# Kernel tuning notes

Measured on AMD Instinct MI355X. Metric: run time of the kernel, lower is better.

Reference implementation:

```python
import jax, jax.numpy as jnp
import numpy as np
from jax import lax

D_MODEL = 60
D_INNER = 120   # expand=2
D_STATE = 16
D_CONV = 4
DT_RANK = 4     # ceil(60/16)
DEPTH = 2
BATCH = 2
H_IMG = 128
W_IMG = 128
L_SEQ = H_IMG * W_IMG


def setup_inputs() -> dict:
    key = jax.random.key(0)
    ks = jax.random.split(key, 12)
    s = 0.02
    x = jax.random.normal(ks[0], (BATCH, L_SEQ, D_MODEL), jnp.float32)
    ln_w = jnp.ones((DEPTH, D_MODEL), jnp.float32)
    ln_b = jnp.zeros((DEPTH, D_MODEL), jnp.float32)
    in_proj_w = jax.random.normal(ks[1], (DEPTH, 2 * D_INNER, D_MODEL), jnp.float32) * s
    conv_w = jax.random.normal(ks[2], (DEPTH, D_INNER, D_CONV), jnp.float32) * s
    conv_b = jnp.zeros((DEPTH, D_INNER), jnp.float32)
    x_proj_w = jax.random.normal(ks[3], (DEPTH, DT_RANK + 2 * D_STATE, D_INNER), jnp.float32) * s
    dt_proj_w = jax.random.normal(ks[4], (DEPTH, D_INNER, DT_RANK), jnp.float32) * s
    dt_proj_b = jnp.full((DEPTH, D_INNER), -4.0, jnp.float32)  # softplus^-1 of small dt
    A_log = jnp.broadcast_to(
        jnp.log(jnp.arange(1, D_STATE + 1, dtype=jnp.float32))[None, None, :],
        (DEPTH, D_INNER, D_STATE)).copy()
    D_skip = jnp.ones((DEPTH, D_INNER), jnp.float32)
    out_proj_w = jax.random.normal(ks[5], (DEPTH, D_MODEL, D_INNER), jnp.float32) * s
    conv2d_w = jax.random.normal(ks[6], (D_MODEL, D_MODEL, 3, 3), jnp.float32) * s
    conv2d_b = jnp.zeros((D_MODEL,), jnp.float32)
    return {"x": x, "ln_w": ln_w, "ln_b": ln_b, "in_proj_w": in_proj_w,
            "conv_w": conv_w, "conv_b": conv_b, "x_proj_w": x_proj_w,
            "dt_proj_w": dt_proj_w, "dt_proj_b": dt_proj_b, "A_log": A_log,
            "D": D_skip, "out_proj_w": out_proj_w,
            "conv2d_w": conv2d_w, "conv2d_b": conv2d_b,
            "H": H_IMG, "W": W_IMG}


def _layernorm(x, w, b, eps=1e-5):
    mu = jnp.mean(x, axis=-1, keepdims=True)
    var = jnp.mean(jnp.square(x - mu), axis=-1, keepdims=True)
    return (x - mu) * lax.rsqrt(var + eps) * w + b


def _selective_scan(dA, dBx, C):
    # dA, dBx: [B, L, D_INNER, D_STATE]; C: [B, L, D_STATE]
    def step(h, inp):
        dA_t, dBx_t, c_t = inp
        h = dA_t * h + dBx_t                       # [B, D_INNER, D_STATE]
        y = jnp.einsum('bdn,bn->bd', h, c_t)
        return h, y
    h0 = jnp.zeros(dA.shape[:1] + dA.shape[2:], dA.dtype)
    _, ys = lax.scan(step, h0,
                     (dA.transpose(1, 0, 2, 3), dBx.transpose(1, 0, 2, 3),
                      C.transpose(1, 0, 2)))
    return ys.transpose(1, 0, 2)                    # [B, L, D_INNER]


def _mamba(x, in_w, cw, cb, xp_w, dtw, dtb, A_log, D_skip, out_w):
    # x: [B, L, D_MODEL]
    xz = jnp.einsum('bld,ed->ble', x, in_w)         # [B, L, 2*D_INNER]
    xin, z = jnp.split(xz, 2, axis=-1)
    # causal depthwise conv1d over L
    xc = xin.transpose(0, 2, 1)                     # [B, D_INNER, L]
    xc = jnp.pad(xc, ((0, 0), (0, 0), (D_CONV - 1, 0)))
    xc = lax.conv_general_dilated(xc, cw[:, None, :], (1,), 'VALID',
                                  dimension_numbers=('NCH', 'OIH', 'NCH'),
                                  feature_group_count=D_INNER)
    xc = jax.nn.silu(xc + cb[None, :, None]).transpose(0, 2, 1)  # [B, L, D_INNER]
    xdb = jnp.einsum('bld,ed->ble', xc, xp_w)       # [B, L, DT_RANK + 2*D_STATE]
    dt = xdb[..., :DT_RANK]
    Bm = xdb[..., DT_RANK:DT_RANK + D_STATE]
    Cm = xdb[..., DT_RANK + D_STATE:]
    delta = jax.nn.softplus(jnp.einsum('blr,dr->bld', dt, dtw) + dtb)  # [B, L, D_INNER]
    A = -jnp.exp(A_log)                              # [D_INNER, D_STATE]
    dA = jnp.exp(delta[..., None] * A[None, None])   # [B, L, D_INNER, D_STATE]
    dBx = delta[..., None] * Bm[:, :, None, :] * xc[..., None]
    y = _selective_scan(dA, dBx, Cm) + D_skip * xc
    y = y * jax.nn.silu(z)
    return jnp.einsum('ble,de->bld', y, out_w)       # [B, L, D_MODEL]


def reference(x, ln_w, ln_b, in_proj_w, conv_w, conv_b, x_proj_w,
              dt_proj_w, dt_proj_b, A_log, D, out_proj_w,
              conv2d_w, conv2d_b, H, W):
    h = x
    for i in range(DEPTH):
        hn = _layernorm(h, ln_w[i], ln_b[i])
        h = _mamba(hn, in_proj_w[i], conv_w[i], conv_b[i], x_proj_w[i],
                   dt_proj_w[i], dt_proj_b[i], A_log[i], D[i], out_proj_w[i])
    # patch_unembed -> 3x3 conv -> patch_embed, residual add (RMMB)
    b = h.shape[0]
    img = h.transpose(0, 2, 1).reshape(b, D_MODEL, H, W)
    img = lax.conv_general_dilated(img, conv2d_w, (1, 1), 'SAME',
                                   dimension_numbers=('NCHW', 'OIHW', 'NCHW'))
    img = img + conv2d_b[None, :, None, None]
    h = img.reshape(b, D_MODEL, H * W).transpose(0, 2, 1)
    return h + x
```

## Files before the change

kernel.cpp:

```cpp
#include <hip/hip_runtime.h>
#include <math.h>

#define BATCH 2
#define LSEQ 16384
#define DM 60
#define DI 120
#define NCH 512
#define TCH 32
#define HH 128
#define WW 128

typedef __attribute__((ext_vector_type(8))) short bhalf8;
typedef __attribute__((ext_vector_type(4))) short short4v;
typedef __attribute__((ext_vector_type(4))) float f32x4;

__device__ __forceinline__ float sigmoidf_(float x){ return __builtin_amdgcn_rcpf(1.0f + __expf(-x)); }
__device__ __forceinline__ float siluf_(float x){ return x * sigmoidf_(x); }
__device__ __forceinline__ float softplusf_(float x){ return (x > 20.0f) ? x : __logf(1.0f + __expf(x)); }
__device__ __forceinline__ short f2b(float f){
  union{float f; unsigned u;} v; v.f = f;
  unsigned r = (v.u + 0x7fffu + ((v.u >> 16) & 1u)) >> 16;
  return (short)r;
}
__device__ __forceinline__ float b2f(short s){
  union{float f; unsigned u;} v; v.u = ((unsigned)(unsigned short)s) << 16; return v.f;
}

__device__ __forceinline__ void powers16(float r, float* dA){
  dA[0] = r;
  #pragma unroll
  for (int n = 1; n < 16; n++) dA[n] = dA[(n-1)>>1] * dA[n>>1];
}
__device__ __forceinline__ void powers8(float r, float* p){
  p[0] = r;
  #pragma unroll
  for (int n = 1; n < 8; n++) p[n] = p[(n-1)>>1] * p[n>>1];
}

__global__ __launch_bounds__(256) void k_pack(
    const float* __restrict__ ipw, const float* __restrict__ xpw,
    const float* __restrict__ opw,
    const float* __restrict__ lnw, const float* __restrict__ lnb,
    short* __restrict__ pk, float* __restrict__ c01)
{
  int i = blockIdx.x*256 + threadIdx.x;
  if (i < 2*240*64){
    int l = i / (240*64);
    int rem = i % (240*64);
    int n = rem / 64, k = rem % 64;
    float v = (k < 60) ? ipw[(size_t)l*14400 + n*60 + k] * lnw[l*60 + k] : 0.f;
    pk[i] = f2b(v);
  } else if (i < 30720 + 2*48*128){
    int j = i - 30720;
    int l = j / (48*128);
    int rem = j % (48*128);
    int n = rem / 128, k = rem % 128;
    float v = (n < 36 && k < 120) ? xpw[(size_t)l*36*120 + n*120 + k] : 0.f;
    pk[i] = f2b(v);
  } else if (i < 43008 + 480){
    int j = i - 43008;
    int l = j / 240, n = j % 240;
    float c1 = 0.f, c0 = 0.f;
    for (int k = 0; k < 60; k++){
      float w = ipw[(size_t)l*14400 + n*60 + k];
      c1 += lnw[l*60+k] * w;
      c0 += lnb[l*60+k] * w;
    }
    c01[(l*240 + n)*2 + 0] = c1;
    c01[(l*240 + n)*2 + 1] = c0;
  } else if (i < 43488 + 2*64*128){
    int j = i - 43488;
    int l = j / 8192;
    int rem = j % 8192;
    int n = rem / 128, k = rem % 128;
    float v = (n < 60 && k < 120) ? opw[(size_t)l*7200 + n*120 + k] : 0.f;
    pk[43008 + j] = f2b(v);
  }
}

__global__ __launch_bounds__(256) void k_lnxp(
    const float* __restrict__ srcf, const short* __restrict__ srcb,
    const short* __restrict__ ipB,
    const float* __restrict__ c01,
    const float* __restrict__ cw, const float* __restrict__ cb,
    const short* __restrict__ xpB,
    const float* __restrict__ dtw, const float* __restrict__ dtb,
    const float* __restrict__ A_log,
    short* __restrict__ zs, short* __restrict__ xcg,
    short* __restrict__ delta, short* __restrict__ BCg,
    float* __restrict__ ap, float* __restrict__ he)
{
  __shared__ __align__(16) char smem[31552];
  short* XB   = (short*)smem;
  short* xcB  = (short*)smem;
  short* xinB = (short*)(smem + 8704);
  float* BLf  = (float*)(smem + 21760);
  short* BCL  = (short*)(smem + 23808);
  float* stats= (float*)(smem + 25856);
  float* dtsh = (float*)(smem + 26240);
  float* cwL  = (float*)(smem + 26752);
  float* Wd5T = (float*)(smem + 28672);
  float* cbL  = (float*)(smem + 30592);
  float* bdL  = (float*)(smem + 31072);
  const int tid = threadIdx.x;
  const int wave = tid >> 6, lane = tid & 63;
  const int m = lane & 15, quad = lane >> 4;
  const int row0 = blockIdx.x * 32;
  const int seq0 = (row0 / LSEQ) * LSEQ;
  for (int i = tid; i < 480; i += 256){ cwL[i] = cw[i]; Wd5T[(i & 3)*120 + (i >> 2)] = dtw[i]; }
  for (int i = tid; i < 120; i += 256){ cbL[i] = cb[i]; bdL[i] = dtb[i]; }
  for (int i = tid; i < 48*16; i += 256){
    int r = i >> 4, g = i & 15;
    int grow = row0 - 3 + r;
    short4v o = {0,0,0,0};
    if (g < 15 && r < 35 && grow >= seq0){
      if (srcb){
        o = *(const short4v*)&srcb[(size_t)grow*60 + g*4];
      } else {
        float4 f = *(const float4*)&srcf[(size_t)grow*60 + g*4];
        o.x = f2b(f.x); o.y = f2b(f.y); o.z = f2b(f.z); o.w = f2b(f.w);
      }
    }
    *(short4v*)&XB[r*72 + g*4] = o;
  }
  __syncthreads();
  {
    const int sub = lane >> 4;
    const int li  = lane & 15;
    #pragma unroll
    for (int it = 0; it < 3; it++){
      int r = it*16 + wave*4 + sub;
      short4v x4 = *(const short4v*)&XB[r*72 + li*4];
      float f0 = b2f(x4.x), f1 = b2f(x4.y), f2 = b2f(x4.z), f3 = b2f(x4.w);
      float sx = (f0 + f1) + (f2 + f3);
      float sq = (f0*f0 + f1*f1) + (f2*f2 + f3*f3);
      #pragma unroll
      for (int off = 1; off < 16; off <<= 1){
        sx += __shfl_xor(sx, off);
        sq += __shfl_xor(sq, off);
      }
      if (li == 0){
        float mu = sx * (1.0f/60.0f);
        float var = fmaxf(sq * (1.0f/60.0f) - mu*mu, 0.f);
        stats[r*2 + 0] = mu;
        stats[r*2 + 1] = rsqrtf(var + 1e-5f);
      }
    }
  }
  __syncthreads();
  for (int t = wave; t < 45; t += 4){
    int mtile = t / 15, ntile = t % 15;
    f32x4 acc = {0.f,0.f,0.f,0.f};
    #pragma unroll
    for (int ks = 0; ks < 2; ks++){
      bhalf8 a = *(const bhalf8*)&XB[(mtile*16 + m)*72 + ks*32 + quad*8];
      bhalf8 b = *(const bhalf8*)&ipB[(ntile*16 + m)*64 + ks*32 + quad*8];
      acc = __builtin_amdgcn_mfma_f32_16x16x32_bf16(a, b, acc, 0, 0, 0);
    }
    int n = ntile*16 + m;
    float2 cc = *(const float2*)&c01[n*2];
    float c1v = cc.x, c0v = cc.y;
    #pragma unroll
    for (int reg = 0; reg < 4; reg++){
      int r = mtile*16 + quad*4 + reg;
      int grow = row0 - 3 + r;
      bool valid = (r < 35) && (grow >= seq0);
      float mu = stats[r*2], rs = stats[r*2+1];
      float val = rs*(acc[reg] - mu*c1v) + c0v;
      if (!valid) val = 0.f;
      if (n < 120){
        xinB[r*136 + n] = f2b(val);
      } else if (r >= 3 && r < 35){
        zs[(size_t)(row0 - 3 + r)*120 + (n - 120)] = f2b(siluf_(val));
      }
    }
  }
  __syncthreads();
  for (int i = tid; i < 960; i += 256){
    int r = i/30, c4 = (i%30)*4;
    float4 cbv = *(const float4*)&cbL[c4];
    float4 w0 = *(const float4*)&cwL[(c4+0)*4];
    float4 w1 = *(const float4*)&cwL[(c4+1)*4];
    float4 w2 = *(const float4*)&cwL[(c4+2)*4];
    float4 w3 = *(const float4*)&cwL[(c4+3)*4];
    short4v x0 = *(const short4v*)&xinB[(r+0)*136 + c4];
    short4v x1 = *(const short4v*)&xinB[(r+1)*136 + c4];
    short4v x2 = *(const short4v*)&xinB[(r+2)*136 + c4];
    short4v x3 = *(const short4v*)&xinB[(r+3)*136 + c4];
    float a0 = cbv.x + w0.x*b2f(x0.x) + w0.y*b2f(x1.x) + w0.z*b2f(x2.x) + w0.w*b2f(x3.x);
    float a1 = cbv.y + w1.x*b2f(x0.y) + w1.y*b2f(x1.y) + w1.z*b2f(x2.y) + w1.w*b2f(x3.y);
    float a2 = cbv.z + w2.x*b2f(x0.z) + w2.y*b2f(x1.z) + w2.z*b2f(x2.z) + w2.w*b2f(x3.z);
    float a3 = cbv.w + w3.x*b2f(x0.w) + w3.y*b2f(x1.w) + w3.z*b2f(x2.w) + w3.w*b2f(x3.w);
    short4v o;
    o.x = f2b(siluf_(a0)); o.y = f2b(siluf_(a1)); o.z = f2b(siluf_(a2)); o.w = f2b(siluf_(a3));
    *(short4v*)&xcB[r*136 + c4] = o;
  }
  for (int i = tid; i < 32*8; i += 256)
    xcB[(i >> 3)*136 + 120 + (i & 7)] = 0;
  __syncthreads();
  for (int t = wave; t < 6; t += 4){
    int mtile = t / 3, ntile = t % 3;
    f32x4 acc = {0.f,0.f,0.f,0.f};
    #pragma unroll
    for (int ks = 0; ks < 4; ks++){
      bhalf8 a = *(const bhalf8*)&xcB[(mtile*16 + m)*136 + ks*32 + quad*8];
      bhalf8 b = *(const bhalf8*)&xpB[(ntile*16 + m)*128 + ks*32 + quad*8];
      acc = __builtin_amdgcn_mfma_f32_16x16x32_bf16(a, b, acc, 0, 0, 0);
    }
    int n = ntile*16 + m;
    #pragma unroll
    for (int reg = 0; reg < 4; reg++){
      int r = mtile*16 + quad*4 + reg;
      float val = acc[reg];
      if (n < 4)        dtsh[r*4 + n] = val;
      else if (n < 36){
        BCL[r*32 + (n - 4)] = f2b(val);
        if (n < 20) BLf[r*16 + (n - 4)] = val;
      }
    }
  }
  __syncthreads();
  for (int i = tid; i < 960; i += 256){
    int row = i/30, c4 = (i%30)*4;
    float4 t4 = *(const float4*)&dtsh[row*4];
    float4 w0 = *(const float4*)&Wd5T[0*120 + c4];
    float4 w1 = *(const float4*)&Wd5T[1*120 + c4];
    float4 w2 = *(const float4*)&Wd5T[2*120 + c4];
    float4 w3 = *(const float4*)&Wd5T[3*120 + c4];
    float4 bb = *(const float4*)&bdL[c4];
    short4v o;
    o.x = f2b(softplusf_(bb.x + t4.x*w0.x + t4.y*w1.x + t4.z*w2.x + t4.w*w3.x));
    o.y = f2b(softplusf_(bb.y + t4.x*w0.y + t4.y*w1.y + t4.z*w2.y + t4.w*w3.y));
    o.z = f2b(softplusf_(bb.z + t4.x*w0.z + t4.y*w1.z + t4.z*w2.z + t4.w*w3.z));
    o.w = f2b(softplusf_(bb.w + t4.x*w0.w + t4.y*w1.w + t4.z*w2.w + t4.w*w3.w));
    *(short4v*)&delta[(size_t)(row0 + row)*120 + c4] = o;
  }
  for (int i = tid; i < 960; i += 256){
    int r = i/30, off = (i%30)*4;
    *(short4v*)&xcg[(size_t)(row0 + r)*120 + off] = *(const short4v*)&xcB[r*136 + off];
  }
  for (int i = tid; i < 256; i += 256)
    *(short4v*)&BCg[(size_t)row0*32 + i*4] = *(const short4v*)&BCL[i*4];
  if (tid < 240){
    const int d = tid >> 1, half = tid & 1, n0 = half*8;
    const int b = row0 / LSEQ;
    const int cglob = (row0 % LSEQ) >> 5;
    float A2[8], h[8];
    const float A20 = -__expf(A_log[d*16]) * 1.44269504f;
    #pragma unroll
    for (int n = 0; n < 8; n++){
      A2[n] = -__expf(A_log[d*16 + n0 + n]) * 1.44269504f;
      h[n] = 0.f;
    }
    bool fastp = true;
    #pragma unroll
    for (int n = 0; n < 8; n++)
      fastp = fastp && (fabsf(A2[n] - (n0+n+1)*A20) <= 1e-4f*fabsf(A2[n]));
    const float w0 = Wd5T[d], w1 = Wd5T[120+d], w2 = Wd5T[240+d], w3 = Wd5T[360+d];
    const float bd = bdL[d];
    int base = (cglob*BATCH + b)*(DI*16) + d*16 + n0;
    if (fastp){
      float P = 1.f;
      for (int t = 0; t < 32; t++){
        float4 t4 = *(const float4*)&dtsh[t*4];
        float del = softplusf_(bd + t4.x*w0 + t4.y*w1 + t4.z*w2 + t4.w*w3);
        float xcv = b2f(xcB[t*136 + d]);
        float dx = del * xcv;
        float r = exp2f(del * A20);
        P *= r;
        float p8[8]; powers8(r, p8);
        float s = half ? p8[7] : 1.0f;
        float4 b0 = *(const float4*)&BLf[t*16 + n0];
        float4 b1 = *(const float4*)&BLf[t*16 + n0 + 4];
        h[0] = (s*p8[0])*h[0] + dx*b0.x;  h[1] = (s*p8[1])*h[1] + dx*b0.y;
        h[2] = (s*p8[2])*h[2] + dx*b0.z;  h[3] = (s*p8[3])*h[3] + dx*b0.w;
        h[4] = (s*p8[4])*h[4] + dx*b1.x;  h[5] = (s*p8[5])*h[5] + dx*b1.y;
        h[6] = (s*p8[6])*h[6] + dx*b1.z;  h[7] = (s*p8[7])*h[7] + dx*b1.w;
      }
      float pp[8]; powers8(P, pp);
      float sP = half ? pp[7] : 1.0f;
      float apv[8];
      #pragma unroll
      for (int j = 0; j < 8; j++) apv[j] = sP*pp[j];
      *(float4*)&ap[base]     = *(float4*)&apv[0];
      *(float4*)&ap[base + 4] = *(float4*)&apv[4];
      *(float4*)&he[base]     = *(float4*)&h[0];
      *(float4*)&he[base + 4] = *(float4*)&h[4];
    } else {
      float apv[8];
      #pragma unroll
      for (int n = 0; n < 8; n++) apv[n] = 1.f;
      for (int t = 0; t < 32; t++){
        float4 t4 = *(const float4*)&dtsh[t*4];
        float del = softplusf_(bd + t4.x*w0 + t4.y*w1 + t4.z*w2 + t4.w*w3);
        float dx = del * b2f(xcB[t*136 + d]);
        #pragma unroll
        for (int n = 0; n < 8; n++){
          float dA = exp2f(del * A2[n]);
          apv[n] *= dA;
          h[n] = dA*h[n] + dx*BLf[t*16 + n0 + n];
        }
      }
      *(float4*)&ap[base]     = *(float4*)&apv[0];
      *(float4*)&ap[base + 4] = *(float4*)&apv[4];
      *(float4*)&he[base]     = *(float4*)&h[0];
      *(float4*)&he[base + 4] = *(float4*)&h[4];
    }
  }
}

__global__ __launch_bounds__(256) void k_scan2(float* __restrict__ ap, const float* __restrict__ he)
{
  __shared__ float aggA[16*17];
  __shared__ float aggB[16*17];
  const int tid = threadIdx.x;
  const int n = tid & 15, j = tid >> 4;
  const int sbase = blockIdx.x*16 + n;
  const int stride = BATCH*DI*16;
  {
    float A = 1.f, B = 0.f;
    int idx = (j*32)*stride + sbase;
    #pragma unroll 4
    for (int k = 0; k < 32; k++){
      float a = ap[idx], h = he[idx];
      B = a*B + h;
      A *= a;
      idx += stride;
    }
    aggA[n*17 + j] = A;
    aggB[n*17 + j] = B;
  }
  __syncthreads();
  if (tid < 16){
    float B = 0.f;
    #pragma unroll
    for (int jj = 0; jj < 16; jj++){
      float Af = aggA[tid*17 + jj];
      float Bf = aggB[tid*17 + jj];
      aggB[tid*17 + jj] = B;
      B = Af*B + Bf;
    }
  }
  __syncthreads();
  {
    float H = aggB[n*17 + j];
    int idx = (j*32)*stride + sbase;
    #pragma unroll 4
    for (int k = 0; k < 32; k++){
      float a = ap[idx], h = he[idx];
      ap[idx] = H;
      H = a*H + h;
      idx += stride;
    }
  }
}

__global__ __launch_bounds__(256) void k_scan3o(
    const short* __restrict__ delta, const short* __restrict__ xc,
    const short* __restrict__ BCg, const short* __restrict__ zs,
    const float* __restrict__ h0, const float* __restrict__ A_log,
    const float* __restrict__ Dsk, const short* __restrict__ opB,
    short* __restrict__ hout)
{
  __shared__ float BCl[TCH*32];
  __shared__ __align__(16) short yL[TCH*136];
  const int tid = threadIdx.x;
  const int wave = tid >> 6, lane = tid & 63;
  const int m = lane & 15, quad = lane >> 4;
  const int c = blockIdx.x % NCH, b = blockIdx.x / NCH;
  const size_t rowbase = (size_t)b*LSEQ + (size_t)c*TCH;
  for (int i = tid; i < TCH*8; i += 256){
    short4v v = *(const short4v*)&BCg[rowbase*32 + i*4];
    float4 f; f.x = b2f(v.x); f.y = b2f(v.y); f.z = b2f(v.z); f.w = b2f(v.w);
    *(float4*)&BCl[i*4] = f;
  }
  for (int i = tid; i < TCH*4; i += 256){
    short4v z = {0,0,0,0};
    *(short4v*)&yL[(i >> 2)*136 + 120 + (i & 3)*4] = z;
  }
  __syncthreads();
  if (tid < 240){
    const int d = tid >> 1, half = tid & 1, n0 = half << 3;
    float A2[8], h[8];
    const int base = (c*BATCH + b)*(DI*16) + d*16 + n0;
    const float A20 = -__expf(A_log[d*16]) * 1.44269504f;
    #pragma unroll
    for (int n = 0; n < 8; n++){
      A2[n] = -__expf(A_log[d*16 + n0 + n]) * 1.44269504f;
      h[n] = h0[base + n];
    }
    bool fastp = true;
    #pragma unroll
    for (int n = 0; n < 8; n++)
      fastp = fastp && (fabsf(A2[n] - (n0+n+1)*A20) <= 1e-4f*fabsf(A2[n]));
    int fp = fastp ? 1 : 0;
    fp &= __shfl_xor(fp, 1);
    const float Dv = Dsk[d];
    if (fp){
      for (int t = 0; t < TCH; t++){
        float del = b2f(delta[(rowbase+t)*DI + d]);
        float xcv = b2f(xc[(rowbase+t)*DI + d]);
        float zv  = b2f(zs[(rowbase+t)*DI + d]);
        float dx = del * xcv;
        float r = exp2f(del * A20);
        float p8[8]; powers8(r, p8);
        float s = half ? p8[7] : 1.0f;
        float4 b0 = *(const float4*)&BCl[t*32 + n0];
        float4 b1 = *(const float4*)&BCl[t*32 + n0 + 4];
        h[0] = (s*p8[0])*h[0] + dx*b0.x;  h[1] = (s*p8[1])*h[1] + dx*b0.y;
        h[2] = (s*p8[2])*h[2] + dx*b0.z;  h[3] = (s*p8[3])*h[3] + dx*b0.w;
        h[4] = (s*p8[4])*h[4] + dx*b1.x;  h[5] = (s*p8[5])*h[5] + dx*b1.y;
        h[6] = (s*p8[6])*h[6] + dx*b1.z;  h[7] = (s*p8[7])*h[7] + dx*b1.w;
        float4 c0 = *(const float4*)&BCl[t*32 + 16 + n0];
        float4 c1 = *(const float4*)&BCl[t*32 + 20 + n0];
        float acc = h[0]*c0.x + h[1]*c0.y + h[2]*c0.z + h[3]*c0.w
                  + h[4]*c1.x + h[5]*c1.y + h[6]*c1.z + h[7]*c1.w;
        acc += __shfl_xor(acc, 1);
        if (!half) yL[t*136 + d] = f2b((acc + Dv*xcv) * zv);
      }
    } else {
      for (int t = 0; t < TCH; t++){
        float del = b2f(delta[(rowbase+t)*DI + d]);
        float xcv = b2f(xc[(rowbase+t)*DI + d]);
        float zv  = b2f(zs[(rowbase+t)*DI + d]);
        float dx = del * xcv;
        float acc = 0.f;
        #pragma unroll
        for (int n = 0; n < 8; n++){
          float dA = exp2f(del * A2[n]);
          h[n] = dA*h[n] + dx*BCl[t*32 + n0 + n];
          acc += h[n]*BCl[t*32 + 16 + n0 + n];
        }
        acc += __shfl_xor(acc, 1);
        if (!half) yL[t*136 + d] = f2b((acc + Dv*xcv) * zv);
      }
    }
  }
  __syncthreads();
  for (int t = wave; t < 8; t += 4){
    const int mtile = t >> 2, ntile = t & 3;
    f32x4 acc = {0.f,0.f,0.f,0.f};
    #pragma unroll
    for (int ks = 0; ks < 4; ks++){
      bhalf8 a  = *(const bhalf8*)&yL[(mtile*16 + m)*136 + ks*32 + quad*8];
      bhalf8 bb = *(const bhalf8*)&opB[(ntile*16 + m)*128 + ks*32 + quad*8];
      acc = __builtin_amdgcn_mfma_f32_16x16x32_bf16(a, bb, acc, 0, 0, 0);
    }
    const int n = ntile*16 + m;
    if (n < 60){
      #pragma unroll
      for (int reg = 0; reg < 4; reg++){
        int r = mtile*16 + quad*4 + reg;
        hout[(rowbase + r)*60 + n] = f2b(acc[reg]);
      }
    }
  }
}

__global__ __launch_bounds__(256) void k_wB(const float* __restrict__ w, short* __restrict__ wB)
{
  int i = blockIdx.x*256 + threadIdx.x;
  if (i >= 9*64*64) return;
  int ci = i & 63, co = (i >> 6) & 63, tap = i >> 12;
  float v = 0.f;
  if (co < 60 && ci < 60) v = w[((size_t)co*60 + ci)*9 + tap];
  wB[i] = f2b(v);
}

__global__ __launch_bounds__(256) void k_conv2d(
    const short* __restrict__ hin, const short* __restrict__ wB,
    const float* __restrict__ cb, const float* __restrict__ xres,
    float* __restrict__ out)
{
  __shared__ short tile[3*66*72];
  const int tid = threadIdx.x;
  const int blk = blockIdx.x;
  const int xhalf = blk & 1;
  const int yy = (blk >> 1) & 127;
  const int b = blk >> 8;
  const int x0 = xhalf*64;
  for (int i = tid; i < 3*66*72; i += 256){
    int ci = i % 72;
    int xx = (i / 72) % 66;
    int row = i / (72*66);
    int gy = yy - 1 + row, gx = x0 - 1 + xx;
    short v = 0;
    if (ci < 60 && gy >= 0 && gy < HH && gx >= 0 && gx < WW)
      v = hin[((size_t)b*LSEQ + gy*WW + gx)*60 + ci];
    tile[i] = v;
  }
  __syncthreads();
  const int wave = tid >> 6, lane = tid & 63;
  const int m = lane & 15, quad = lane >> 4;
  f32x4 acc0 = {0.f,0.f,0.f,0.f}, acc1 = {0.f,0.f,0.f,0.f};
  f32x4 acc2 = {0.f,0.f,0.f,0.f}, acc3 = {0.f,0.f,0.f,0.f};
  #pragma unroll
  for (int tap = 0; tap < 9; tap++){
    const int ky = tap/3, kx = tap%3;
    const short* arow = &tile[(ky*66 + wave*16 + m + kx)*72];
    const short* brow = wB + tap*4096;
    #pragma unroll
    for (int kh = 0; kh < 2; kh++){
      const int k0 = kh*32 + quad*8;
      bhalf8 a = *(const bhalf8*)(arow + k0);
      bhalf8 b0 = *(const bhalf8*)(brow + (0*16 + m)*64 + k0);
      bhalf8 b1 = *(const bhalf8*)(brow + (1*16 + m)*64 + k0);
      bhalf8 b2 = *(const bhalf8*)(brow + (2*16 + m)*64 + k0);
      bhalf8 b3 = *(const bhalf8*)(brow + (3*16 + m)*64 + k0);
      acc0 = __builtin_amdgcn_mfma_f32_16x16x32_bf16(a, b0, acc0, 0, 0, 0);
      acc1 = __builtin_amdgcn_mfma_f32_16x16x32_bf16(a, b1, acc1, 0, 0, 0);
      acc2 = __builtin_amdgcn_mfma_f32_16x16x32_bf16(a, b2, acc2, 0, 0, 0);
      acc3 = __builtin_amdgcn_mfma_f32_16x16x32_bf16(a, b3, acc3, 0, 0, 0);
    }
  }
  const size_t rowb = (size_t)b*LSEQ + yy*WW + x0;
  f32x4 accs[4] = {acc0, acc1, acc2, acc3};
  #pragma unroll
  for (int nt = 0; nt < 4; nt++){
    int co = nt*16 + m;
    if (co < 60){
      float bias = cb[co];
      #pragma unroll
      for (int reg = 0; reg < 4; reg++){
        int px = wave*16 + quad*4 + reg;
        size_t o = (rowb + px)*60 + co;
        out[o] = accs[nt][reg] + bias + xres[o];
      }
    }
  }
}

extern "C" void kernel_launch(void* const* d_in, const int* in_sizes, int n_in,
                              void* d_out, int out_size, void* d_ws, size_t ws_size,
                              hipStream_t stream)
{
  const float* x      = (const float*)d_in[0];
  const float* ln_w   = (const float*)d_in[1];
  const float* ln_b   = (const float*)d_in[2];
  const float* ipw    = (const float*)d_in[3];
  const float* cw     = (const float*)d_in[4];
  const float* cb1    = (const float*)d_in[5];
  const float* xpw    = (const float*)d_in[6];
  const float* dtw    = (const float*)d_in[7];
  const float* dtb    = (const float*)d_in[8];
  const float* A_log  = (const float*)d_in[9];
  const float* Dsk    = (const float*)d_in[10];
  const float* opw    = (const float*)d_in[11];
  const float* c2w    = (const float*)d_in[12];
  const float* c2b    = (const float*)d_in[13];
  float* out = (float*)d_out;

  char* ws = (char*)d_ws;
  size_t off = 0;
  short* zsb   = (short*)(ws + off); off += (size_t)BATCH*LSEQ*DI*2;
  short* xcb   = (short*)(ws + off); off += (size_t)BATCH*LSEQ*DI*2;
  short* dlt   = (short*)(ws + off); off += (size_t)BATCH*LSEQ*DI*2;
  short* BCg   = (short*)(ws + off); off += (size_t)BATCH*LSEQ*32*2;
  float* apb   = (float*)(ws + off); off += (size_t)NCH*BATCH*DI*16*4;
  float* heb   = (float*)(ws + off); off += (size_t)NCH*BATCH*DI*16*4;
  short* hcur  = (short*)(ws + off); off += (size_t)BATCH*LSEQ*DM*2;
  short* wBb   = (short*)(ws + off); off += (size_t)9*64*64*2;
  short* pkb   = (short*)(ws + off); off += (size_t)(2*240*64 + 2*48*128 + 2*64*128)*2;
  float* c01b  = (float*)(ws + off); off += (size_t)2*240*2*4;

  const int rows = BATCH*LSEQ;
  k_pack<<<(43008 + 480 + 16384 + 255)/256, 256, 0, stream>>>(ipw, xpw, opw, ln_w, ln_b, pkb, c01b);
  for (int layer = 0; layer < 2; layer++){
    const float* srcf = (layer == 0) ? x : nullptr;
    const short* srcb = (layer == 0) ? nullptr : hcur;
    k_lnxp<<<rows/32, 256, 0, stream>>>(srcf, srcb,
                                        pkb + (size_t)layer*240*64,
                                        c01b + (size_t)layer*240*2,
                                        cw + layer*DI*4, cb1 + layer*DI,
                                        pkb + 30720 + (size_t)layer*48*128,
                                        dtw + (size_t)layer*DI*4, dtb + layer*DI,
                                        A_log + (size_t)layer*DI*16,
                                        zsb, xcb, dlt, BCg, apb, heb);
    k_scan2<<<BATCH*DI, 256, 0, stream>>>(apb, heb);
    k_scan3o<<<BATCH*NCH, 256, 0, stream>>>(dlt, xcb, BCg, zsb, apb, A_log + (size_t)layer*DI*16,
                                            Dsk + layer*DI, pkb + 43008 + (size_t)layer*8192, hcur);
  }
  k_wB<<<(9*64*64+255)/256, 256, 0, stream>>>(c2w, wBb);
  k_conv2d<<<BATCH*HH*2, 256, 0, stream>>>(hcur, wBb, c2b, x, out);
}
```

Measured before the change: 290.6 us.

## Widen lnxp to 512 threads, reuse staged delta in chunk scan, vectorize conv2d tile load

The fused LN/in-proj/conv/x-proj kernel now launches with 512 threads. The per-chunk scan is split across 480 threads, each owning 4 states instead of 8, with a wave-shuffle vote for the fast path. The scan now reads delta staged in shared memory instead of recomputing softplus per state group, which adds one extra barrier. Separately, the conv2d halo tile load uses 4-wide short vectors instead of scalar loads. The larger blocks may lower occupancy, and shared memory is reused for the delta buffer.

```diff
diff --git a/kernel.cpp b/kernel.cpp
--- a/kernel.cpp
+++ b/kernel.cpp
@@ -78,7 +78,7 @@
   }
 }
 
-__global__ __launch_bounds__(256) void k_lnxp(
+__global__ __launch_bounds__(512) void k_lnxp(
     const float* __restrict__ srcf, const short* __restrict__ srcb,
     const short* __restrict__ ipB,
     const float* __restrict__ c01,
@@ -94,6 +94,7 @@
   short* XB   = (short*)smem;
   short* xcB  = (short*)smem;
   short* xinB = (short*)(smem + 8704);
+  short* delL = (short*)(smem + 8704);
   float* BLf  = (float*)(smem + 21760);
   short* BCL  = (short*)(smem + 23808);
   float* stats= (float*)(smem + 25856);
@@ -107,9 +108,9 @@
   const int m = lane & 15, quad = lane >> 4;
   const int row0 = blockIdx.x * 32;
   const int seq0 = (row0 / LSEQ) * LSEQ;
-  for (int i = tid; i < 480; i += 256){ cwL[i] = cw[i]; Wd5T[(i & 3)*120 + (i >> 2)] = dtw[i]; }
-  for (int i = tid; i < 120; i += 256){ cbL[i] = cb[i]; bdL[i] = dtb[i]; }
-  for (int i = tid; i < 48*16; i += 256){
+  if (tid < 480){ cwL[tid] = cw[tid]; Wd5T[(tid & 3)*120 + (tid >> 2)] = dtw[tid]; }
+  if (tid < 120){ cbL[tid] = cb[tid]; bdL[tid] = dtb[tid]; }
+  for (int i = tid; i < 48*16; i += 512){
     int r = i >> 4, g = i & 15;
     int grow = row0 - 3 + r;
     short4v o = {0,0,0,0};
@@ -128,27 +129,29 @@
     const int sub = lane >> 4;
     const int li  = lane & 15;
     #pragma unroll
-    for (int it = 0; it < 3; it++){
-      int r = it*16 + wave*4 + sub;
-      short4v x4 = *(const short4v*)&XB[r*72 + li*4];
-      float f0 = b2f(x4.x), f1 = b2f(x4.y), f2 = b2f(x4.z), f3 = b2f(x4.w);
-      float sx = (f0 + f1) + (f2 + f3);
-      float sq = (f0*f0 + f1*f1) + (f2*f2 + f3*f3);
-      #pragma unroll
-      for (int off = 1; off < 16; off <<= 1){
-        sx += __shfl_xor(sx, off);
-        sq += __shfl_xor(sq, off);
-      }
-      if (li == 0){
-        float mu = sx * (1.0f/60.0f);
-        float var = fmaxf(sq * (1.0f/60.0f) - mu*mu, 0.f);
-        stats[r*2 + 0] = mu;
-        stats[r*2 + 1] = rsqrtf(var + 1e-5f);
-      }
-    }
-  }
-  __syncthreads();
-  for (int t = wave; t < 45; t += 4){
+    for (int it = 0; it < 2; it++){
+      int r = it*32 + wave*4 + sub;
+      if (r < 48){
+        short4v x4 = *(const short4v*)&XB[r*72 + li*4];
+        float f0 = b2f(x4.x), f1 = b2f(x4.y), f2 = b2f(x4.z), f3 = b2f(x4.w);
+        float sx = (f0 + f1) + (f2 + f3);
+        float sq = (f0*f0 + f1*f1) + (f2*f2 + f3*f3);
+        #pragma unroll
+        for (int off = 1; off < 16; off <<= 1){
+          sx += __shfl_xor(sx, off);
+          sq += __shfl_xor(sq, off);
+        }
+        if (li == 0){
+          float mu = sx * (1.0f/60.0f);
+          float var = fmaxf(sq * (1.0f/60.0f) - mu*mu, 0.f);
+          stats[r*2 + 0] = mu;
+          stats[r*2 + 1] = rsqrtf(var + 1e-5f);
+        }
+      }
+    }
+  }
+  __syncthreads();
+  for (int t = wave; t < 45; t += 8){
     int mtile = t / 15, ntile = t % 15;
     f32x4 acc = {0.f,0.f,0.f,0.f};
     #pragma unroll
@@ -176,7 +179,7 @@
     }
   }
   __syncthreads();
-  for (int i = tid; i < 960; i += 256){
+  for (int i = tid; i < 960; i += 512){
     int r = i/30, c4 = (i%30)*4;
     float4 cbv = *(const float4*)&cbL[c4];
     float4 w0 = *(const float4*)&cwL[(c4+0)*4];
@@ -195,10 +198,10 @@
     o.x = f2b(siluf_(a0)); o.y = f2b(siluf_(a1)); o.z = f2b(siluf_(a2)); o.w = f2b(siluf_(a3));
     *(short4v*)&xcB[r*136 + c4] = o;
   }
-  for (int i = tid; i < 32*8; i += 256)
+  for (int i = tid; i < 32*8; i += 512)
     xcB[(i >> 3)*136 + 120 + (i & 7)] = 0;
   __syncthreads();
-  for (int t = wave; t < 6; t += 4){
+  for (int t = wave; t < 6; t += 8){
     int mtile = t / 3, ntile = t % 3;
     f32x4 acc = {0.f,0.f,0.f,0.f};
     #pragma unroll
@@ -220,7 +223,7 @@
     }
   }
   __syncthreads();
-  for (int i = tid; i < 960; i += 256){
+  for (int i = tid; i < 960; i += 512){
     int row = i/30, c4 = (i%30)*4;
     float4 t4 = *(const float4*)&dtsh[row*4];
     float4 w0 = *(const float4*)&Wd5T[0*120 + c4];
@@ -233,78 +236,75 @@
     o.y = f2b(softplusf_(bb.y + t4.x*w0.y + t4.y*w1.y + t4.z*w2.y + t4.w*w3.y));
     o.z = f2b(softplusf_(bb.z + t4.x*w0.z + t4.y*w1.z + t4.z*w2.z + t4.w*w3.z));
     o.w = f2b(softplusf_(bb.w + t4.x*w0.w + t4.y*w1.w + t4.z*w2.w + t4.w*w3.w));
+    *(short4v*)&delL[row*120 + c4] = o;
     *(short4v*)&delta[(size_t)(row0 + row)*120 + c4] = o;
   }
-  for (int i = tid; i < 960; i += 256){
+  __syncthreads();
+  for (int i = tid; i < 960; i += 512){
     int r = i/30, off = (i%30)*4;
     *(short4v*)&xcg[(size_t)(row0 + r)*120 + off] = *(const short4v*)&xcB[r*136 + off];
   }
-  for (int i = tid; i < 256; i += 256)
+  for (int i = tid; i < 256; i += 512)
     *(short4v*)&BCg[(size_t)row0*32 + i*4] = *(const short4v*)&BCL[i*4];
-  if (tid < 240){
-    const int d = tid >> 1, half = tid & 1, n0 = half*8;
+  if (tid < 480){
+    const int d = tid >> 2, q = tid & 3, n0 = q << 2;
     const int b = row0 / LSEQ;
     const int cglob = (row0 % LSEQ) >> 5;
-    float A2[8], h[8];
+    float A2[4], h[4];
     const float A20 = -__expf(A_log[d*16]) * 1.44269504f;
     #pragma unroll
-    for (int n = 0; n < 8; n++){
+    for (int n = 0; n < 4; n++){
       A2[n] = -__expf(A_log[d*16 + n0 + n]) * 1.44269504f;
       h[n] = 0.f;
     }
     bool fastp = true;
     #pragma unroll
-    for (int n = 0; n < 8; n++)
+    for (int n = 0; n < 4; n++)
       fastp = fastp && (fabsf(A2[n] - (n0+n+1)*A20) <= 1e-4f*fabsf(A2[n]));
-    const float w0 = Wd5T[d], w1 = Wd5T[120+d], w2 = Wd5T[240+d], w3 = Wd5T[360+d];
-    const float bd = bdL[d];
+    int fp = fastp ? 1 : 0;
+    fp &= __shfl_xor(fp, 1);
+    fp &= __shfl_xor(fp, 2);
     int base = (cglob*BATCH + b)*(DI*16) + d*16 + n0;
-    if (fastp){
+    if (fp){
       float P = 1.f;
+      const int sh1 = q & 1, sh2 = q & 2;
       for (int t = 0; t < 32; t++){
-        float4 t4 = *(const float4*)&dtsh[t*4];
-        float del = softplusf_(bd + t4.x*w0 + t4.y*w1 + t4.z*w2 + t4.w*w3);
+        float del = b2f(delL[t*120 + d]);
         float xcv = b2f(xcB[t*136 + d]);
         float dx = del * xcv;
         float r = exp2f(del * A20);
         P *= r;
-        float p8[8]; powers8(r, p8);
-        float s = half ? p8[7] : 1.0f;
-        float4 b0 = *(const float4*)&BLf[t*16 + n0];
-        float4 b1 = *(const float4*)&BLf[t*16 + n0 + 4];
-        h[0] = (s*p8[0])*h[0] + dx*b0.x;  h[1] = (s*p8[1])*h[1] + dx*b0.y;
-        h[2] = (s*p8[2])*h[2] + dx*b0.z;  h[3] = (s*p8[3])*h[3] + dx*b0.w;
-        h[4] = (s*p8[4])*h[4] + dx*b1.x;  h[5] = (s*p8[5])*h[5] + dx*b1.y;
-        h[6] = (s*p8[6])*h[6] + dx*b1.z;  h[7] = (s*p8[7])*h[7] + dx*b1.w;
-      }
-      float pp[8]; powers8(P, pp);
-      float sP = half ? pp[7] : 1.0f;
-      float apv[8];
-      #pragma unroll
-      for (int j = 0; j < 8; j++) apv[j] = sP*pp[j];
-      *(float4*)&ap[base]     = *(float4*)&apv[0];
-      *(float4*)&ap[base + 4] = *(float4*)&apv[4];
-      *(float4*)&he[base]     = *(float4*)&h[0];
-      *(float4*)&he[base + 4] = *(float4*)&h[4];
+        float p1 = r*r;
+        float p2 = p1*r, p3 = p1*p1;
+        float s = sh1 ? p3 : 1.0f;
+        if (sh2) s *= p3*p3;
+        float4 bv = *(const float4*)&BLf[t*16 + n0];
+        h[0] = (s*r )*h[0] + dx*bv.x;
+        h[1] = (s*p1)*h[1] + dx*bv.y;
+        h[2] = (s*p2)*h[2] + dx*bv.z;
+        h[3] = (s*p3)*h[3] + dx*bv.w;
+      }
+      float P1 = P*P;
+      float P2 = P1*P, P3 = P1*P1;
+      float sP = sh1 ? P3 : 1.0f;
+      if (sh2) sP *= P3*P3;
+      float apv[4] = {sP*P, sP*P1, sP*P2, sP*P3};
+      *(float4*)&ap[base] = *(float4*)&apv[0];
+      *(float4*)&he[base] = *(float4*)&h[0];
     } else {
-      float apv[8];
-      #pragma unroll
-      for (int n = 0; n < 8; n++) apv[n] = 1.f;
+      float apv[4] = {1.f,1.f,1.f,1.f};
       for (int t = 0; t < 32; t++){
-        float4 t4 = *(const float4*)&dtsh[t*4];
-        float del = softplusf_(bd + t4.x*w0 + t4.y*w1 + t4.z*w2 + t4.w*w3);
+        float del = b2f(delL[t*120 + d]);
         float dx = del * b2f(xcB[t*136 + d]);
         #pragma unroll
-        for (int n = 0; n < 8; n++){
+        for (int n = 0; n < 4; n++){
           float dA = exp2f(del * A2[n]);
           apv[n] *= dA;
           h[n] = dA*h[n] + dx*BLf[t*16 + n0 + n];
         }
       }
-      *(float4*)&ap[base]     = *(float4*)&apv[0];
-      *(float4*)&ap[base + 4] = *(float4*)&apv[4];
-      *(float4*)&he[base]     = *(float4*)&h[0];
-      *(float4*)&he[base + 4] = *(float4*)&h[4];
+      *(float4*)&ap[base] = *(float4*)&apv[0];
+      *(float4*)&he[base] = *(float4*)&h[0];
     }
   }
 }
@@ -479,15 +479,15 @@
   const int yy = (blk >> 1) & 127;
   const int b = blk >> 8;
   const int x0 = xhalf*64;
-  for (int i = tid; i < 3*66*72; i += 256){
-    int ci = i % 72;
-    int xx = (i / 72) % 66;
-    int row = i / (72*66);
+  for (int i = tid; i < 3*66*18; i += 256){
+    int g = i % 18;
+    int xx = (i / 18) % 66;
+    int row = i / (18*66);
     int gy = yy - 1 + row, gx = x0 - 1 + xx;
-    short v = 0;
-    if (ci < 60 && gy >= 0 && gy < HH && gx >= 0 && gx < WW)
-      v = hin[((size_t)b*LSEQ + gy*WW + gx)*60 + ci];
-    tile[i] = v;
+    short4v v = {0,0,0,0};
+    if (g < 15 && gy >= 0 && gy < HH && gx >= 0 && gx < WW)
+      v = *(const short4v*)&hin[((size_t)b*LSEQ + gy*WW + gx)*60 + g*4];
+    *(short4v*)&tile[(row*66 + xx)*72 + g*4] = v;
   }
   __syncthreads();
   const int wave = tid >> 6, lane = tid & 63;
@@ -568,7 +568,7 @@
   for (int layer = 0; layer < 2; layer++){
     const float* srcf = (layer == 0) ? x : nullptr;
     const short* srcb = (layer == 0) ? nullptr : hcur;
-    k_lnxp<<<rows/32, 256, 0, stream>>>(srcf, srcb,
+    k_lnxp<<<rows/32, 512, 0, stream>>>(srcf, srcb,
                                         pkb + (size_t)layer*240*64,
                                         c01b + (size_t)layer*240*2,
                                         cw + layer*DI*4, cb1 + layer*DI,
```

After: 277.6 us. 1.05x faster.
